# Performance work log

Hardware: AMD Instinct MI355X
Metric: run time of the kernel (lower is better)

Reference implementation:

```python
import jax, jax.numpy as jnp
import numpy as np

EPS = 1e-6

def ln(x):
    m = jnp.mean(x, axis=-1, keepdims=True)
    v = jnp.var(x, axis=-1, keepdims=True)
    return (x - m) * jax.lax.rsqrt(v + EPS)

def modulate(x, shift, scale):
    return x * (1.0 + scale[:, None, :]) + shift[:, None, :]

def setup_inputs() -> dict:
    key = jax.random.key(0)
    ks = jax.random.split(key, 16)
    B, N, H = 2, 384, 256
    D = 128  # n_vector_features * scale_dist_features
    MIN = 2 * H + D  # 640
    FH = 1024  # swiglu_correction_fn(4.0, 256)
    s = 0.02
    inp = {
        "mask": jnp.ones((B, N), jnp.float32),
        "x": jax.random.normal(ks[0], (B, N, H), jnp.float32),
        "t_emb": jax.random.normal(ks[1], (B, H), jnp.float32),
        "dist": jax.random.normal(ks[2], (B, N, N, D), jnp.float32),
        "edge_mask": jnp.ones((B, N, N), jnp.float32),
        "W_ada": jax.random.normal(ks[3], (6 * H, H), jnp.float32) * s,
        "b_ada": jnp.zeros((6 * H,), jnp.float32),
        "W_fe1": jax.random.normal(ks[4], (H, MIN), jnp.float32) * s,
        "b_fe1": jnp.zeros((H,), jnp.float32),
        "W_fe2": jax.random.normal(ks[5], (H, H), jnp.float32) * s,
        "b_fe2": jnp.zeros((H,), jnp.float32),
        "W_qkv": jax.random.normal(ks[6], (3 * H, H), jnp.float32) * s,
        "W_out": jax.random.normal(ks[7], (H, H), jnp.float32) * s,
        "W_ffn1": jax.random.normal(ks[8], (2 * FH, H), jnp.float32) * s,
        "W_ffn2": jax.random.normal(ks[9], (H, FH), jnp.float32) * s,
    }
    return inp

def reference(mask, x, t_emb, dist, edge_mask, W_ada, b_ada, W_fe1, b_fe1,
              W_fe2, b_fe2, W_qkv, W_out, W_ffn1, W_ffn2):
    B, N, H = x.shape
    num_heads = 8
    d_head = H // num_heads
    mN = mask[..., None]  # (B,N,1)

    # adaLN modulation
    ada = jax.nn.silu(t_emb) @ W_ada.T + b_ada  # (B,6H)
    shift_msa, scale_msa, gate_msa, shift_mlp, scale_mlp, gate_mlp = jnp.split(ada, 6, axis=1)

    x_norm = modulate(ln(x * mN), shift_msa, scale_msa)  # (B,N,H)

    # all-pairs message passing: concat(h_i, h_j, dist_ij) -> MLP -> sum_j
    h1 = jnp.broadcast_to(x_norm[:, :, None, :], (B, N, N, H))
    h2 = jnp.broadcast_to(x_norm[:, None, :, :], (B, N, N, H))
    feats = jnp.concatenate([h1, h2, dist], axis=-1) * edge_mask[..., None]
    msgs = jax.nn.silu(feats @ W_fe1.T + b_fe1) @ W_fe2.T + b_fe2  # (B,N,N,H)
    x_msg = jnp.sum(msgs, axis=-2)  # (B,N,H)

    # attention
    qkv = x_msg @ W_qkv.T
    Q, K, V = jnp.split(qkv, 3, axis=-1)
    Q = ln(Q * mN)
    K = ln(K * mN)
    def heads(t):
        return t.reshape(B, N, num_heads, d_head).transpose(0, 2, 1, 3)  # b h s d
    Q, K, V = heads(Q), heads(K), heads(V)
    scores = jnp.einsum("bhqd,bhkd->bhqk", Q, K) / jnp.sqrt(jnp.float32(d_head))
    bias = jnp.where(mask[:, None, None, :] > 0, 0.0, -1e9)
    attn = jax.nn.softmax(scores + bias, axis=-1)
    ao = jnp.einsum("bhqk,bhkd->bhqd", attn, V)
    ao = ao.transpose(0, 2, 1, 3).reshape(B, N, H)
    y = ao @ W_out.T

    x = x + gate_msa[:, None, :] * y

    # SwiGLU FFN
    xm = modulate(ln(x * mN), shift_mlp, scale_mlp)
    h12 = xm @ W_ffn1.T
    h_a, h_b = jnp.split(h12, 2, axis=-1)
    ffn_out = (jax.nn.silu(h_a) * h_b) @ W_ffn2.T
    x = (x + gate_mlp[:, None, :] * ffn_out) * mN
    return x
```

## Files before the change

### kernel.cpp

```cpp
#include <hip/hip_runtime.h>

#define DEVI __device__ __forceinline__

typedef float fv4 __attribute__((ext_vector_type(4)));
typedef __bf16 bf16x8 __attribute__((ext_vector_type(8)));
typedef unsigned short u16x8 __attribute__((ext_vector_type(8)));
typedef unsigned short u16x4 __attribute__((ext_vector_type(4)));

DEVI fv4 ldv4(const float* p) { return *reinterpret_cast<const fv4*>(p); }
DEVI bf16x8 pkbf(fv4 a, fv4 b) {
  bf16x8 r;
  r[0] = (__bf16)a[0]; r[1] = (__bf16)a[1]; r[2] = (__bf16)a[2]; r[3] = (__bf16)a[3];
  r[4] = (__bf16)b[0]; r[5] = (__bf16)b[1]; r[6] = (__bf16)b[2]; r[7] = (__bf16)b[3];
  return r;
}
DEVI u16x8 b2u(bf16x8 v) { return __builtin_bit_cast(u16x8, v); }
DEVI bf16x8 asbf(u16x8 u) { return __builtin_bit_cast(bf16x8, u); }
DEVI unsigned short bfbits(float x) { __bf16 v = (__bf16)x; return __builtin_bit_cast(unsigned short, v); }
DEVI u16x4 pk4(fv4 a) {
  u16x4 u;
  u[0] = bfbits(a[0]); u[1] = bfbits(a[1]); u[2] = bfbits(a[2]); u[3] = bfbits(a[3]);
  return u;
}
DEVI fv4 MFMA16(bf16x8 a, bf16x8 b, fv4 c) {
  return __builtin_amdgcn_mfma_f32_16x16x32_bf16(a, b, c, 0, 0, 0);
}
DEVI float siluf(float x) {
  float e = __builtin_amdgcn_exp2f(x * -1.44269504f);
  return x * __builtin_amdgcn_rcpf(1.f + e);
}
DEVI fv4 glu4(fv4 x, fv4 y) {
  fv4 r;
#pragma unroll
  for (int j = 0; j < 4; ++j) r[j] = siluf(x[j]) * y[j];
  return r;
}
DEVI void lbar() {
  asm volatile("s_waitcnt lgkmcnt(0)" ::: "memory");
  __builtin_amdgcn_s_barrier();
}
DEVI int swz(int row, int k) {
  int unit = k >> 3;
  int phys = (unit & ~7) | ((unit ^ row) & 7);
  return row * 384 + (phys << 3) + (k & 7);
}

__global__ __launch_bounds__(256)
void k_ada(const float* __restrict__ temb, const float* __restrict__ W_ada,
           const float* __restrict__ b_ada, float* __restrict__ ada) {
  __shared__ float sm[256];
  const int b = blockIdx.x / 6;
  const int r = (blockIdx.x % 6) * 256 + threadIdx.x;
  sm[threadIdx.x] = siluf(temb[b * 256 + threadIdx.x]);
  __syncthreads();
  float s = b_ada[r];
  const float* wr = W_ada + (size_t)r * 256;
  for (int k = 0; k < 256; ++k) s += sm[k] * wr[k];
  ada[b * 1536 + r] = s;
}

__global__ __launch_bounds__(256)
void k_xnorm(const float* __restrict__ xin, const float* __restrict__ mask,
             const float* __restrict__ ada, int shift_off, int scale_off,
             float* __restrict__ out) {
  const int row = blockIdx.x;
  const int b = row / 384;
  const int t = threadIdx.x;
  const float m = mask[row];
  const float v = xin[(size_t)row * 256 + t] * m;
  float s = v, ss = v * v;
#pragma unroll
  for (int o = 1; o < 64; o <<= 1) { s += __shfl_xor(s, o); ss += __shfl_xor(ss, o); }
  __shared__ float red[8];
  const int wid = t >> 6;
  if ((t & 63) == 0) { red[wid] = s; red[4 + wid] = ss; }
  __syncthreads();
  s = red[0] + red[1] + red[2] + red[3];
  ss = red[4] + red[5] + red[6] + red[7];
  const float mean = s * (1.f / 256.f);
  const float var = ss * (1.f / 256.f) - mean * mean;
  const float rs = rsqrtf(var + 1e-6f);
  out[(size_t)row * 256 + t] =
      (v - mean) * rs * (1.f + ada[b * 1536 + scale_off + t]) + ada[b * 1536 + shift_off + t];
}

template <int EPI, int AMODE>
__global__ __launch_bounds__(256)
void k_gemm(const float* __restrict__ A, int lda,
            const float* __restrict__ B, int ldb, int koff, int K,
            float* __restrict__ C, int ldc,
            const float* __restrict__ bias, float bscale,
            const float* __restrict__ res,
            const float* __restrict__ ada, int gate_off,
            const float* __restrict__ mask) {
  __shared__ __align__(16) unsigned short As[64 * 64];
  __shared__ __align__(16) unsigned short Bs[64 * 64];
  const int t = threadIdx.x, lane = t & 63, w = t >> 6;
  const int bn0 = blockIdx.x * 64, bm0 = blockIdx.y * 64;
  const int qr = (w >> 1) * 32, qc = (w & 1) * 32;
  const int g = lane >> 4, c = lane & 15;
  const int srow = t >> 2;
  const int so = (t & 3) * 2;
  const int o0 = so ^ (srow & 7), o1 = (so + 1) ^ (srow & 7);
  unsigned short* aw0 = As + srow * 64 + o0 * 8;
  unsigned short* aw1 = As + srow * 64 + o1 * 8;
  unsigned short* bw0 = Bs + srow * 64 + o0 * 8;
  unsigned short* bw1 = Bs + srow * 64 + o1 * 8;
  const float* ag = A + (size_t)(bm0 + srow) * lda + so * 8;
  const int vrow = bn0 + srow;
  const float* bg;
  if constexpr (EPI == 7)
    bg = B + (size_t)(vrow & 255) * ldb + (vrow >> 8) * 256 + so * 8;
  else
    bg = B + (size_t)vrow * ldb + koff + so * 8;
  const float* a2g = nullptr;
  if constexpr (AMODE == 2) a2g = res + ((size_t)(bm0 + srow) * lda + so * 8);
  fv4 a0 = ldv4(ag), a1 = ldv4(ag + 4), a2 = ldv4(ag + 8), a3 = ldv4(ag + 12);
  fv4 x0, x1, x2, x3;
  if constexpr (AMODE == 1) {
    x0 = ldv4(ag + 1024); x1 = ldv4(ag + 1028); x2 = ldv4(ag + 1032); x3 = ldv4(ag + 1036);
  }
  if constexpr (AMODE == 2) {
    x0 = ldv4(a2g); x1 = ldv4(a2g + 4); x2 = ldv4(a2g + 8); x3 = ldv4(a2g + 12);
  }
  fv4 c0 = ldv4(bg), c1 = ldv4(bg + 4), c2 = ldv4(bg + 8), c3 = ldv4(bg + 12);
  fv4 acc[2][2] = {};
  for (int k0 = 0; k0 < K; k0 += 64) {
    lbar();
    if constexpr (AMODE == 1) {
      *reinterpret_cast<u16x8*>(aw0) = b2u(pkbf(glu4(a0, x0), glu4(a1, x1)));
      *reinterpret_cast<u16x8*>(aw1) = b2u(pkbf(glu4(a2, x2), glu4(a3, x3)));
    } else if constexpr (AMODE == 2) {
      *reinterpret_cast<u16x8*>(aw0) = b2u(pkbf(a0 + x0, a1 + x1));
      *reinterpret_cast<u16x8*>(aw1) = b2u(pkbf(a2 + x2, a3 + x3));
    } else {
      *reinterpret_cast<u16x8*>(aw0) = b2u(pkbf(a0, a1));
      *reinterpret_cast<u16x8*>(aw1) = b2u(pkbf(a2, a3));
    }
    *reinterpret_cast<u16x8*>(bw0) = b2u(pkbf(c0, c1));
    *reinterpret_cast<u16x8*>(bw1) = b2u(pkbf(c2, c3));
    lbar();
    if (k0 + 64 < K) {
      ag += 64; bg += 64;
      a0 = ldv4(ag); a1 = ldv4(ag + 4); a2 = ldv4(ag + 8); a3 = ldv4(ag + 12);
      if constexpr (AMODE == 1) {
        x0 = ldv4(ag + 1024); x1 = ldv4(ag + 1028); x2 = ldv4(ag + 1032); x3 = ldv4(ag + 1036);
      }
      if constexpr (AMODE == 2) {
        a2g += 64;
        x0 = ldv4(a2g); x1 = ldv4(a2g + 4); x2 = ldv4(a2g + 8); x3 = ldv4(a2g + 12);
      }
      c0 = ldv4(bg); c1 = ldv4(bg + 4); c2 = ldv4(bg + 8); c3 = ldv4(bg + 12);
    }
#pragma unroll
    for (int kk = 0; kk < 2; ++kk) {
      bf16x8 af[2], bf[2];
#pragma unroll
      for (int mi = 0; mi < 2; ++mi) {
        int row = qr + mi * 16 + c;
        int oct = (kk * 4 + g) ^ (row & 7);
        af[mi] = asbf(*reinterpret_cast<const u16x8*>(As + row * 64 + oct * 8));
      }
#pragma unroll
      for (int ni = 0; ni < 2; ++ni) {
        int row = qc + ni * 16 + c;
        int oct = (kk * 4 + g) ^ (row & 7);
        bf[ni] = asbf(*reinterpret_cast<const u16x8*>(Bs + row * 64 + oct * 8));
      }
#pragma unroll
      for (int mi = 0; mi < 2; ++mi)
#pragma unroll
        for (int ni = 0; ni < 2; ++ni)
          acc[mi][ni] = MFMA16(af[mi], bf[ni], acc[mi][ni]);
    }
  }
#pragma unroll
  for (int mi = 0; mi < 2; ++mi)
#pragma unroll
    for (int ni = 0; ni < 2; ++ni)
#pragma unroll
      for (int r = 0; r < 4; ++r) {
        int row = bm0 + qr + mi * 16 + g * 4 + r;
        int col = bn0 + qc + ni * 16 + c;
        float v = acc[mi][ni][r];
        if constexpr (EPI == 7) {
          if (col < 256) {
            C[(size_t)row * ldc + col] = v;
          } else {
            int cq = col - 256;
            size_t idx = (((size_t)(row >> 4) * 8 + (cq >> 5)) * 64 +
                          ((row >> 2) & 3) * 16 + (cq & 15)) * 8 +
                         ((cq >> 4) & 1) * 4 + (row & 3);
            ((float*)res)[idx] = v;
          }
        } else {
          if constexpr (EPI == 1) v += bscale * bias[col];
          if constexpr (EPI == 2) v = res[(size_t)row * 256 + col] + ada[(row / 384) * 1536 + gate_off + col] * v;
          if constexpr (EPI == 3) v = (res[(size_t)row * 256 + col] + ada[(row / 384) * 1536 + gate_off + col] * v) * mask[row];
          C[(size_t)row * ldc + col] = v;
        }
      }
}

__global__ __launch_bounds__(512)
void k_edge(const float* __restrict__ dist, const float* __restrict__ emask,
            const float* __restrict__ Wfe1, const float* __restrict__ bfe1,
            const float* __restrict__ P, const float* __restrict__ Qx,
            float* __restrict__ S0, float* __restrict__ S1) {
  const int blk = blockIdx.x, jh = blockIdx.y;
  const int b = blk / 384, i = blk - b * 384;
  const int t = threadIdx.x, lane = t & 63, w = t >> 6;
  const int g = lane >> 4, c = lane & 15;
  __shared__ __align__(16) unsigned short Al[2][16 * 128];

  bf16x8 Bf[2][4];
  float Pl[2], bl[2], Ss[2] = {0.f, 0.f};
#pragma unroll
  for (int ht = 0; ht < 2; ++ht) {
    const int h = w * 32 + ht * 16 + c;
    const float* wp = Wfe1 + (size_t)h * 640 + 512 + g * 8;
#pragma unroll
    for (int ks = 0; ks < 4; ++ks)
      Bf[ht][ks] = pkbf(ldv4(wp + ks * 32), ldv4(wp + ks * 32 + 4));
    Pl[ht] = P[(size_t)(b * 384 + i) * 256 + h];
    bl[ht] = bfe1[h];
  }
  const float* dbase = dist + (size_t)(b * 384 + i) * 49152 + (size_t)jh * 24576;
  const float* embase = emask + (size_t)(b * 384 + i) * 384 + jh * 192;
  const int jcb = b * 24 + jh * 12;
  const float* qbase = Qx + (((size_t)jcb * 8 + w) * 64 + lane) * 8;

  const int srow = t >> 5, kq = t & 31;
  const int sunit = kq >> 1;
  const int sphys = (sunit & 8) | ((sunit ^ (srow & 7)) & 7);
  const int soff = srow * 128 + sphys * 8 + (kq & 1) * 4;

  fv4 rX, rY, qvX0, qvX1, qvY0, qvY1, emX, emY;
  {
    fv4 t0 = ldv4(dbase + t * 4);
    *reinterpret_cast<u16x4*>(&Al[0][soff]) = pk4(t0);
  }
  rX = ldv4(dbase + 2048 + t * 4);
  qvX0 = ldv4(qbase);
  qvX1 = ldv4(qbase + 4);
  emX = ldv4(embase + g * 4);
  lbar();

#pragma unroll 1
  for (int p = 0; p < 6; ++p) {
    {
      const int cl = 2 * p;
      if (cl <= 9) rY = ldv4(dbase + (size_t)(cl + 2) * 2048 + t * 4);
      if (cl <= 10) {
        *reinterpret_cast<u16x4*>(&Al[1][soff]) = pk4(rX);
        const float* qp = qbase + (size_t)(cl + 1) * 4096;
        qvY0 = ldv4(qp);
        qvY1 = ldv4(qp + 4);
        emY = ldv4(embase + (cl + 1) * 16 + g * 4);
      }
      fv4 acc0, acc1;
#pragma unroll
      for (int r = 0; r < 4; ++r) { acc0[r] = Pl[0] + qvX0[r]; acc1[r] = Pl[1] + qvX1[r]; }
#pragma unroll
      for (int ks = 0; ks < 4; ++ks) {
        const int u = ks * 4 + g;
        const int phys = (u & 8) | ((u ^ (c & 7)) & 7);
        bf16x8 af = asbf(*reinterpret_cast<const u16x8*>(&Al[0][c * 128 + phys * 8]));
        acc0 = MFMA16(af, Bf[0][ks], acc0);
        acc1 = MFMA16(af, Bf[1][ks], acc1);
      }
#pragma unroll
      for (int r = 0; r < 4; ++r) {
        Ss[0] += siluf(emX[r] * acc0[r] + bl[0]);
        Ss[1] += siluf(emX[r] * acc1[r] + bl[1]);
      }
      lbar();
    }
    {
      const int cl = 2 * p + 1;
      if (cl <= 9) rX = ldv4(dbase + (size_t)(cl + 2) * 2048 + t * 4);
      if (cl <= 10) {
        *reinterpret_cast<u16x4*>(&Al[0][soff]) = pk4(rY);
        const float* qp = qbase + (size_t)(cl + 1) * 4096;
        qvX0 = ldv4(qp);
        qvX1 = ldv4(qp + 4);
        emX = ldv4(embase + (cl + 1) * 16 + g * 4);
      }
      fv4 acc0, acc1;
#pragma unroll
      for (int r = 0; r < 4; ++r) { acc0[r] = Pl[0] + qvY0[r]; acc1[r] = Pl[1] + qvY1[r]; }
#pragma unroll
      for (int ks = 0; ks < 4; ++ks) {
        const int u = ks * 4 + g;
        const int phys = (u & 8) | ((u ^ (c & 7)) & 7);
        bf16x8 af = asbf(*reinterpret_cast<const u16x8*>(&Al[1][c * 128 + phys * 8]));
        acc0 = MFMA16(af, Bf[0][ks], acc0);
        acc1 = MFMA16(af, Bf[1][ks], acc1);
      }
#pragma unroll
      for (int r = 0; r < 4; ++r) {
        Ss[0] += siluf(emY[r] * acc0[r] + bl[0]);
        Ss[1] += siluf(emY[r] * acc1[r] + bl[1]);
      }
      lbar();
    }
  }
  float* Sp = jh ? S1 : S0;
#pragma unroll
  for (int ht = 0; ht < 2; ++ht) {
    float s = Ss[ht];
    s += __shfl_xor(s, 16);
    s += __shfl_xor(s, 32);
    if (g == 0) Sp[(size_t)(b * 384 + i) * 256 + w * 32 + ht * 16 + c] = s;
  }
}

__global__ __launch_bounds__(256)
void k_lnqk(const float* __restrict__ qkv, const float* __restrict__ mask,
            float* __restrict__ Qn, float* __restrict__ Kn) {
  const int row = blockIdx.x, t = threadIdx.x;
  const float m = mask[row];
  const float q = qkv[(size_t)row * 768 + t] * m;
  const float k = qkv[(size_t)row * 768 + 256 + t] * m;
  float sq = q, sqq = q * q, sk = k, skk = k * k;
#pragma unroll
  for (int o = 1; o < 64; o <<= 1) {
    sq += __shfl_xor(sq, o); sqq += __shfl_xor(sqq, o);
    sk += __shfl_xor(sk, o); skk += __shfl_xor(skk, o);
  }
  __shared__ float red[16];
  const int wid = t >> 6;
  if ((t & 63) == 0) { red[wid] = sq; red[4 + wid] = sqq; red[8 + wid] = sk; red[12 + wid] = skk; }
  __syncthreads();
  sq = red[0] + red[1] + red[2] + red[3];
  sqq = red[4] + red[5] + red[6] + red[7];
  sk = red[8] + red[9] + red[10] + red[11];
  skk = red[12] + red[13] + red[14] + red[15];
  const float mq = sq * (1.f / 256.f), vq = sqq * (1.f / 256.f) - mq * mq;
  const float mk = sk * (1.f / 256.f), vk = skk * (1.f / 256.f) - mk * mk;
  Qn[(size_t)row * 256 + t] = (q - mq) * rsqrtf(vq + 1e-6f);
  Kn[(size_t)row * 256 + t] = (k - mk) * rsqrtf(vk + 1e-6f);
}

__global__ __launch_bounds__(256)
void k_attn(const float* __restrict__ Qn, const float* __restrict__ Kn,
            const float* __restrict__ qkv, const float* __restrict__ mask,
            float* __restrict__ ao) {
  const int bh = blockIdx.y, b = bh >> 3, h = bh & 7;
  const int qg = blockIdx.x;
  const int t = threadIdx.x, lane = t & 63, w = t >> 6;
  const int g = lane >> 4, c = lane & 15;
  __shared__ __align__(16) unsigned short Vt[32 * 384];
  __shared__ __align__(16) unsigned short pl[16 * 384];
  __shared__ float outp[4][16][32];
  __shared__ float redm[4][16], reds[4][16];
  {
    const int d0 = (t & 7) * 4;
    const int kp = t >> 3;
#pragma unroll
    for (int pass = 0; pass < 6; ++pass) {
      int k = pass * 64 + kp * 2;
      fv4 v0 = ldv4(qkv + (size_t)(b * 384 + k) * 768 + 512 + h * 32 + d0);
      fv4 v1 = ldv4(qkv + (size_t)(b * 384 + k + 1) * 768 + 512 + h * 32 + d0);
#pragma unroll
      for (int j = 0; j < 4; ++j) {
        int d = d0 + j;
        unsigned int pr = (unsigned int)bfbits(v0[j]) | ((unsigned int)bfbits(v1[j]) << 16);
        *reinterpret_cast<unsigned int*>(&Vt[swz(d, k)]) = pr;
      }
    }
  }
  bf16x8 qf;
  {
    const float* qp = Qn + (size_t)(b * 384 + qg * 16 + c) * 256 + h * 32 + g * 8;
    qf = pkbf(ldv4(qp), ldv4(qp + 4));
  }
  fv4 sc[6];
#pragma unroll
  for (int kb = 0; kb < 6; ++kb) {
    const float* kp2 = Kn + (size_t)(b * 384 + w * 96 + kb * 16 + c) * 256 + h * 32 + g * 8;
    bf16x8 kf = pkbf(ldv4(kp2), ldv4(kp2 + 4));
    fv4 z = {0.f, 0.f, 0.f, 0.f};
    sc[kb] = MFMA16(qf, kf, z);
  }
  const float rs = 0.1767766952966369f;
  float zz[6][4], mx[4] = {-3e38f, -3e38f, -3e38f, -3e38f};
#pragma unroll
  for (int kb = 0; kb < 6; ++kb) {
    float mb = mask[b * 384 + w * 96 + kb * 16 + c] > 0.f ? 0.f : -1e9f;
#pragma unroll
    for (int r = 0; r < 4; ++r) {
      zz[kb][r] = sc[kb][r] * rs + mb;
      mx[r] = fmaxf(mx[r], zz[kb][r]);
    }
  }
#pragma unroll
  for (int r = 0; r < 4; ++r) {
#pragma unroll
    for (int o = 1; o < 16; o <<= 1) mx[r] = fmaxf(mx[r], __shfl_xor(mx[r], o));
  }
  if (c == 0) {
#pragma unroll
    for (int r = 0; r < 4; ++r) redm[w][g * 4 + r] = mx[r];
  }
  __syncthreads();
  float m4[4], sm[4] = {0.f, 0.f, 0.f, 0.f};
#pragma unroll
  for (int r = 0; r < 4; ++r) {
    int q = g * 4 + r;
    m4[r] = fmaxf(fmaxf(redm[0][q], redm[1][q]), fmaxf(redm[2][q], redm[3][q]));
  }
#pragma unroll
  for (int kb = 0; kb < 6; ++kb) {
    int k = w * 96 + kb * 16 + c;
#pragma unroll
    for (int r = 0; r < 4; ++r) {
      float p = __builtin_amdgcn_exp2f((zz[kb][r] - m4[r]) * 1.44269504f);
      sm[r] += p;
      pl[swz(g * 4 + r, k)] = bfbits(p);
    }
  }
#pragma unroll
  for (int r = 0; r < 4; ++r) {
#pragma unroll
    for (int o = 1; o < 16; o <<= 1) sm[r] += __shfl_xor(sm[r], o);
  }
  if (c == 0) {
#pragma unroll
    for (int r = 0; r < 4; ++r) reds[w][g * 4 + r] = sm[r];
  }
  __syncthreads();
  fv4 oacc[2] = {};
#pragma unroll
  for (int kk = 0; kk < 3; ++kk) {
    int kbase = w * 96 + kk * 32 + g * 8;
    bf16x8 pa = asbf(*reinterpret_cast<const u16x8*>(&pl[swz(c, kbase)]));
#pragma unroll
    for (int db = 0; db < 2; ++db) {
      int d = db * 16 + c;
      bf16x8 vb = asbf(*reinterpret_cast<const u16x8*>(&Vt[swz(d, kbase)]));
      oacc[db] = MFMA16(pa, vb, oacc[db]);
    }
  }
#pragma unroll
  for (int db = 0; db < 2; ++db)
#pragma unroll
    for (int r = 0; r < 4; ++r) outp[w][g * 4 + r][db * 16 + c] = oacc[db][r];
  __syncthreads();
#pragma unroll
  for (int idx = t; idx < 512; idx += 256) {
    int q = idx >> 5, d = idx & 31;
    float v = outp[0][q][d] + outp[1][q][d] + outp[2][q][d] + outp[3][q][d];
    float s = reds[0][q] + reds[1][q] + reds[2][q] + reds[3][q];
    ao[(size_t)(b * 384 + qg * 16 + q) * 256 + h * 32 + d] = v / s;
  }
}

extern "C" void kernel_launch(void* const* d_in, const int* in_sizes, int n_in,
                              void* d_out, int out_size, void* d_ws, size_t ws_size,
                              hipStream_t stream) {
  (void)in_sizes; (void)n_in; (void)out_size; (void)ws_size;
  const float* mask   = (const float*)d_in[0];
  const float* x      = (const float*)d_in[1];
  const float* temb   = (const float*)d_in[2];
  const float* dist   = (const float*)d_in[3];
  const float* emask  = (const float*)d_in[4];
  const float* W_ada  = (const float*)d_in[5];
  const float* b_ada  = (const float*)d_in[6];
  const float* W_fe1  = (const float*)d_in[7];
  const float* b_fe1  = (const float*)d_in[8];
  const float* W_fe2  = (const float*)d_in[9];
  const float* b_fe2  = (const float*)d_in[10];
  const float* W_qkv  = (const float*)d_in[11];
  const float* W_out  = (const float*)d_in[12];
  const float* W_ffn1 = (const float*)d_in[13];
  const float* W_ffn2 = (const float*)d_in[14];
  float* out = (float*)d_out;
  float* ws = (float*)d_ws;

  float* ada   = ws;
  float* xattn = ws + 4096;
  float* xm    = ws + 200704;
  float* xn    = ws + 397312;
  float* P     = ws + 593920;
  float* Qx    = ws + 790528;
  float* S0    = ws + 987136;
  float* xmsg  = ws + 1183744;
  float* qkvb  = ws + 1380352;
  float* Qn    = ws + 1970176;
  float* Kn    = ws + 2166784;
  float* aob   = ws + 2363392;
  float* S1    = ws + 2363392;
  float* h12   = ws + 397312;

  k_ada<<<12, 256, 0, stream>>>(temb, W_ada, b_ada, ada);
  k_xnorm<<<768, 256, 0, stream>>>(x, mask, ada, 0, 256, xn);
  k_gemm<7, 0><<<dim3(8, 12), 256, 0, stream>>>(xn, 256, W_fe1, 640, 0, 256, P, 256,
                                                nullptr, 0.f, Qx, nullptr, 0, nullptr);
  k_edge<<<dim3(768, 2), 512, 0, stream>>>(dist, emask, W_fe1, b_fe1, P, Qx, S0, S1);
  k_gemm<1, 2><<<dim3(4, 12), 256, 0, stream>>>(S0, 256, W_fe2, 256, 0, 256, xmsg, 256,
                                                b_fe2, 384.f, S1, nullptr, 0, nullptr);
  k_gemm<0, 0><<<dim3(12, 12), 256, 0, stream>>>(xmsg, 256, W_qkv, 256, 0, 256, qkvb, 768,
                                                 nullptr, 0.f, nullptr, nullptr, 0, nullptr);
  k_lnqk<<<768, 256, 0, stream>>>(qkvb, mask, Qn, Kn);
  k_attn<<<dim3(24, 16), 256, 0, stream>>>(Qn, Kn, qkvb, mask, aob);
  k_gemm<2, 0><<<dim3(4, 12), 256, 0, stream>>>(aob, 256, W_out, 256, 0, 256, xattn, 256,
                                                nullptr, 0.f, x, ada, 512, nullptr);
  k_xnorm<<<768, 256, 0, stream>>>(xattn, mask, ada, 768, 1024, xm);
  k_gemm<0, 0><<<dim3(32, 12), 256, 0, stream>>>(xm, 256, W_ffn1, 256, 0, 256, h12, 2048,
                                                 nullptr, 0.f, nullptr, nullptr, 0, nullptr);
  k_gemm<3, 1><<<dim3(4, 12), 256, 0, stream>>>(h12, 2048, W_ffn2, 1024, 0, 1024, out, 256,
                                                nullptr, 0.f, xattn, ada, 1280, mask);
}
```

Measured before the change: 141.9 us.

## Fuse Q/K layernorm into QKV GEMM epilogue stats and attention prologue

Removes the separate k_lnqk kernel. The QKV GEMM epilogue now writes per-row partial sums and sums-of-squares for each 64-column tile, and the attention kernel uses them to normalize Q and K from the raw qkv buffer as it loads them. The edge kernel's block index is also remapped so that consecutive blocks interleave rows across the grid. This saves one launch and the Qn/Kn round trip through memory, at the cost of extra per-tile reductions and a shared-memory sync inside the GEMM.

```diff
diff --git a/kernel.cpp b/kernel.cpp
--- a/kernel.cpp
+++ b/kernel.cpp
@@ -200,6 +200,34 @@
           C[(size_t)row * ldc + col] = v;
         }
       }
+  if constexpr (EPI == 8) {
+    if (bn0 < 512) {
+      __shared__ float sred[2][64][2];
+#pragma unroll
+      for (int mi = 0; mi < 2; ++mi)
+#pragma unroll
+        for (int r = 0; r < 4; ++r) {
+          int lrow = qr + mi * 16 + g * 4 + r;
+          float m = mask[bm0 + lrow];
+          float ps = 0.f, pss = 0.f;
+#pragma unroll
+          for (int ni = 0; ni < 2; ++ni) {
+            float vv = acc[mi][ni][r] * m;
+            ps += vv; pss += vv * vv;
+          }
+#pragma unroll
+          for (int o = 1; o < 16; o <<= 1) { ps += __shfl_xor(ps, o); pss += __shfl_xor(pss, o); }
+          if (c == 0) { sred[w & 1][lrow][0] = ps; sred[w & 1][lrow][1] = pss; }
+        }
+      __syncthreads();
+      if (t < 64) {
+        float s = sred[0][t][0] + sred[1][t][0];
+        float ss = sred[0][t][1] + sred[1][t][1];
+        float* st = (float*)res + (size_t)(bm0 + t) * 16 + (bn0 >> 6) * 2;
+        st[0] = s; st[1] = ss;
+      }
+    }
+  }
 }
 
 __global__ __launch_bounds__(512)
@@ -207,7 +235,8 @@
             const float* __restrict__ Wfe1, const float* __restrict__ bfe1,
             const float* __restrict__ P, const float* __restrict__ Qx,
             float* __restrict__ S0, float* __restrict__ S1) {
-  const int blk = blockIdx.x, jh = blockIdx.y;
+  const int obx = blockIdx.x, jh = blockIdx.y;
+  const int blk = (obx & 7) * 96 + (obx >> 3);
   const int b = blk / 384, i = blk - b * 384;
   const int t = threadIdx.x, lane = t & 63, w = t >> 6;
   const int g = lane >> 4, c = lane & 15;
@@ -316,36 +345,8 @@
 }
 
 __global__ __launch_bounds__(256)
-void k_lnqk(const float* __restrict__ qkv, const float* __restrict__ mask,
-            float* __restrict__ Qn, float* __restrict__ Kn) {
-  const int row = blockIdx.x, t = threadIdx.x;
-  const float m = mask[row];
-  const float q = qkv[(size_t)row * 768 + t] * m;
-  const float k = qkv[(size_t)row * 768 + 256 + t] * m;
-  float sq = q, sqq = q * q, sk = k, skk = k * k;
-#pragma unroll
-  for (int o = 1; o < 64; o <<= 1) {
-    sq += __shfl_xor(sq, o); sqq += __shfl_xor(sqq, o);
-    sk += __shfl_xor(sk, o); skk += __shfl_xor(skk, o);
-  }
-  __shared__ float red[16];
-  const int wid = t >> 6;
-  if ((t & 63) == 0) { red[wid] = sq; red[4 + wid] = sqq; red[8 + wid] = sk; red[12 + wid] = skk; }
-  __syncthreads();
-  sq = red[0] + red[1] + red[2] + red[3];
-  sqq = red[4] + red[5] + red[6] + red[7];
-  sk = red[8] + red[9] + red[10] + red[11];
-  skk = red[12] + red[13] + red[14] + red[15];
-  const float mq = sq * (1.f / 256.f), vq = sqq * (1.f / 256.f) - mq * mq;
-  const float mk = sk * (1.f / 256.f), vk = skk * (1.f / 256.f) - mk * mk;
-  Qn[(size_t)row * 256 + t] = (q - mq) * rsqrtf(vq + 1e-6f);
-  Kn[(size_t)row * 256 + t] = (k - mk) * rsqrtf(vk + 1e-6f);
-}
-
-__global__ __launch_bounds__(256)
-void k_attn(const float* __restrict__ Qn, const float* __restrict__ Kn,
-            const float* __restrict__ qkv, const float* __restrict__ mask,
-            float* __restrict__ ao) {
+void k_attn(const float* __restrict__ qkv, const float* __restrict__ stats,
+            const float* __restrict__ mask, float* __restrict__ ao) {
   const int bh = blockIdx.y, b = bh >> 3, h = bh & 7;
   const int qg = blockIdx.x;
   const int t = threadIdx.x, lane = t & 63, w = t >> 6;
@@ -354,6 +355,7 @@
   __shared__ __align__(16) unsigned short pl[16 * 384];
   __shared__ float outp[4][16][32];
   __shared__ float redm[4][16], reds[4][16];
+  __shared__ float kst[384][2];
   {
     const int d0 = (t & 7) * 4;
     const int kp = t >> 3;
@@ -370,16 +372,51 @@
       }
     }
   }
+  for (int idx = t; idx < 384; idx += 256) {
+    const float* sp = stats + (size_t)(b * 384 + idx) * 16 + 8;
+    fv4 s0 = ldv4(sp), s1 = ldv4(sp + 4);
+    float sum = s0[0] + s0[2] + s1[0] + s1[2];
+    float ssq = s0[1] + s0[3] + s1[1] + s1[3];
+    float mean = sum * (1.f / 256.f);
+    kst[idx][0] = mean;
+    kst[idx][1] = rsqrtf(ssq * (1.f / 256.f) - mean * mean + 1e-6f);
+  }
   bf16x8 qf;
   {
-    const float* qp = Qn + (size_t)(b * 384 + qg * 16 + c) * 256 + h * 32 + g * 8;
-    qf = pkbf(ldv4(qp), ldv4(qp + 4));
-  }
+    const int qrow = b * 384 + qg * 16 + c;
+    const float* sp = stats + (size_t)qrow * 16;
+    fv4 s0 = ldv4(sp), s1 = ldv4(sp + 4);
+    float sum = s0[0] + s0[2] + s1[0] + s1[2];
+    float ssq = s0[1] + s0[3] + s1[1] + s1[3];
+    float mq = sum * (1.f / 256.f);
+    float rsq = rsqrtf(ssq * (1.f / 256.f) - mq * mq + 1e-6f);
+    float qm = mask[qrow];
+    const float* qp = qkv + (size_t)qrow * 768 + h * 32 + g * 8;
+    fv4 q0 = ldv4(qp), q1 = ldv4(qp + 4);
+#pragma unroll
+    for (int j = 0; j < 4; ++j) {
+      q0[j] = (q0[j] * qm - mq) * rsq;
+      q1[j] = (q1[j] * qm - mq) * rsq;
+    }
+    qf = pkbf(q0, q1);
+  }
+  __syncthreads();
   fv4 sc[6];
+  float kmb[6];
 #pragma unroll
   for (int kb = 0; kb < 6; ++kb) {
-    const float* kp2 = Kn + (size_t)(b * 384 + w * 96 + kb * 16 + c) * 256 + h * 32 + g * 8;
-    bf16x8 kf = pkbf(ldv4(kp2), ldv4(kp2 + 4));
+    const int krow = w * 96 + kb * 16 + c;
+    const float km = mask[b * 384 + krow];
+    kmb[kb] = km;
+    const float kmean = kst[krow][0], krstd = kst[krow][1];
+    const float* kp2 = qkv + (size_t)(b * 384 + krow) * 768 + 256 + h * 32 + g * 8;
+    fv4 k0 = ldv4(kp2), k1 = ldv4(kp2 + 4);
+#pragma unroll
+    for (int j = 0; j < 4; ++j) {
+      k0[j] = (k0[j] * km - kmean) * krstd;
+      k1[j] = (k1[j] * km - kmean) * krstd;
+    }
+    bf16x8 kf = pkbf(k0, k1);
     fv4 z = {0.f, 0.f, 0.f, 0.f};
     sc[kb] = MFMA16(qf, kf, z);
   }
@@ -387,7 +424,7 @@
   float zz[6][4], mx[4] = {-3e38f, -3e38f, -3e38f, -3e38f};
 #pragma unroll
   for (int kb = 0; kb < 6; ++kb) {
-    float mb = mask[b * 384 + w * 96 + kb * 16 + c] > 0.f ? 0.f : -1e9f;
+    float mb = kmb[kb] > 0.f ? 0.f : -1e9f;
 #pragma unroll
     for (int r = 0; r < 4; ++r) {
       zz[kb][r] = sc[kb][r] * rs + mb;
@@ -487,9 +524,8 @@
   float* S0    = ws + 987136;
   float* xmsg  = ws + 1183744;
   float* qkvb  = ws + 1380352;
-  float* Qn    = ws + 1970176;
-  float* Kn    = ws + 2166784;
-  float* aob   = ws + 2363392;
+  float* stats = ws + 1970176;
+  float* aob   = ws + 2166784;
   float* S1    = ws + 2363392;
   float* h12   = ws + 397312;
 
@@ -500,10 +536,9 @@
   k_edge<<<dim3(768, 2), 512, 0, stream>>>(dist, emask, W_fe1, b_fe1, P, Qx, S0, S1);
   k_gemm<1, 2><<<dim3(4, 12), 256, 0, stream>>>(S0, 256, W_fe2, 256, 0, 256, xmsg, 256,
                                                 b_fe2, 384.f, S1, nullptr, 0, nullptr);
-  k_gemm<0, 0><<<dim3(12, 12), 256, 0, stream>>>(xmsg, 256, W_qkv, 256, 0, 256, qkvb, 768,
-                                                 nullptr, 0.f, nullptr, nullptr, 0, nullptr);
-  k_lnqk<<<768, 256, 0, stream>>>(qkvb, mask, Qn, Kn);
-  k_attn<<<dim3(24, 16), 256, 0, stream>>>(Qn, Kn, qkvb, mask, aob);
+  k_gemm<8, 0><<<dim3(12, 12), 256, 0, stream>>>(xmsg, 256, W_qkv, 256, 0, 256, qkvb, 768,
+                                                 nullptr, 0.f, stats, nullptr, 0, mask);
+  k_attn<<<dim3(24, 16), 256, 0, stream>>>(qkvb, stats, mask, aob);
   k_gemm<2, 0><<<dim3(4, 12), 256, 0, stream>>>(aob, 256, W_out, 256, 0, 256, xattn, 256,
                                                 nullptr, 0.f, x, ada, 512, nullptr);
   k_xnorm<<<768, 256, 0, stream>>>(xattn, mask, ada, 768, 1024, xm);
```

After: 141.6 us (median of 2 runs). Within noise of the previous version (-0.2%).
